# Performance work log

Hardware: AMD Instinct MI355X
Metric: run time of the kernel (lower is better)

The kernel has to match this reference:

```python
import jax, jax.numpy as jnp
import numpy as np

B, S, D, H = 2, 2048, 1024, 16
DK = D // H  # 64


def _quantum(x, W1, b1, W2, b2):
    # Stand-in for QuantumNeuralLayer: classical->quantum->classical, d_k -> d_k.
    return jnp.tanh(x @ W1 + b1) @ W2 + b2


def setup_inputs() -> dict:
    key = jax.random.key(0)
    ks = jax.random.split(key, 16)
    s = 1.0 / np.sqrt(DK)
    inp = {
        "q": jax.random.normal(ks[0], (B, S, D), dtype=jnp.float32),
        "k": jax.random.normal(ks[1], (B, S, D), dtype=jnp.float32),
        "v": jax.random.normal(ks[2], (B, S, D), dtype=jnp.float32),
    }
    names = ["q", "k", "v"]
    for i, n in enumerate(names):
        inp[f"W{n}1"] = jax.random.normal(ks[3 + 4 * i], (DK, DK), dtype=jnp.float32) * s
        inp[f"b{n}1"] = jnp.zeros((DK,), dtype=jnp.float32)
        inp[f"W{n}2"] = jax.random.normal(ks[4 + 4 * i], (DK, DK), dtype=jnp.float32) * s
        inp[f"b{n}2"] = jnp.zeros((DK,), dtype=jnp.float32)
    inp["Wo"] = jax.random.normal(ks[15], (D, D), dtype=jnp.float32) * (1.0 / np.sqrt(D))
    inp["bo"] = jnp.zeros((D,), dtype=jnp.float32)
    return inp


def reference(q, k, v, Wq1, bq1, Wq2, bq2, Wk1, bk1, Wk2, bk2,
              Wv1, bv1, Wv2, bv2, Wo, bo):
    b, s, _ = q.shape
    # split heads: [B, S, H, DK]
    qh = q.reshape(b, s, H, DK)
    kh = k.reshape(b, s, H, DK)
    vh = v.reshape(b, s, H, DK)
    # quantum per-feature transform on last dim
    qh = _quantum(qh, Wq1, bq1, Wq2, bq2)
    kh = _quantum(kh, Wk1, bk1, Wk2, bk2)
    vh = _quantum(vh, Wv1, bv1, Wv2, bv2)
    scale = 1.0 / jnp.sqrt(jnp.asarray(DK, dtype=qh.dtype))
    # scores: [B, H, S, S]
    scores = jnp.einsum("bqhd,bkhd->bhqk", qh, kh) * scale
    attn = jax.nn.softmax(scores, axis=-1)
    # context: [B, H, S, DK] -> [B, S, D]
    ctx = jnp.einsum("bhqk,bkhd->bqhd", attn, vh).reshape(b, s, D)
    return ctx @ Wo + bo
```

## Files before the change

### kernel.cpp

```cpp
#include <hip/hip_runtime.h>

#define B_ 2
#define S_ 2048
#define D_ 1024
#define H_ 16
#define DK_ 64

typedef float f32x4 __attribute__((ext_vector_type(4)));
typedef float f32x16 __attribute__((ext_vector_type(16)));
typedef short bf16x8 __attribute__((ext_vector_type(8)));

static __device__ __forceinline__ unsigned short f2bf(float f) {
  unsigned u = __float_as_uint(f);
  unsigned r = (u + 0x7FFFu + ((u >> 16) & 1u)) >> 16;
  return (unsigned short)r;
}

static __device__ __forceinline__ unsigned cvtpk_bf16(float lo, float hi) {
  unsigned r;
  asm("v_cvt_pk_bf16_f32 %0, %1, %2" : "=v"(r) : "v"(lo), "v"(hi));
  return r;
}

static __device__ __forceinline__ void load16_lds(const void* g, void* lds) {
  __builtin_amdgcn_global_load_lds(
      (const __attribute__((address_space(1))) unsigned int*)g,
      (__attribute__((address_space(3))) unsigned int*)lds, 16, 0, 0);
}

static __device__ __forceinline__ bf16x8 make_pa8(const float* p, int hi) {
  unsigned x1 = cvtpk_bf16(p[0], p[1]);
  unsigned x2 = cvtpk_bf16(p[2], p[3]);
  unsigned y1 = cvtpk_bf16(p[4], p[5]);
  unsigned y2 = cvtpk_bf16(p[6], p[7]);
  unsigned sx1 = (unsigned)__shfl_xor((int)x1, 32);
  unsigned sx2 = (unsigned)__shfl_xor((int)x2, 32);
  unsigned sy1 = (unsigned)__shfl_xor((int)y1, 32);
  unsigned sy2 = (unsigned)__shfl_xor((int)y2, 32);
  union {
    unsigned u[4];
    bf16x8 v;
  } pa;
  pa.u[0] = hi ? sy1 : x1;
  pa.u[1] = hi ? sy2 : x2;
  pa.u[2] = hi ? y1 : sx1;
  pa.u[3] = hi ? y2 : sx2;
  return pa.v;
}

static __device__ __forceinline__ float tanh_fast(float x) {
  float xc = fminf(fmaxf(x, -9.0f), 9.0f);
  float e = exp2f(xc * 2.88539008177792681472f);
  return (e - 1.0f) / (e + 1.0f);
}

__global__ __launch_bounds__(256) void quantum_fused(
    const float* __restrict__ xq, const float* __restrict__ xk,
    const float* __restrict__ xv,
    const float* __restrict__ Wq1, const float* __restrict__ bq1,
    const float* __restrict__ Wq2, const float* __restrict__ bq2,
    const float* __restrict__ Wk1, const float* __restrict__ bk1,
    const float* __restrict__ Wk2, const float* __restrict__ bk2,
    const float* __restrict__ Wv1, const float* __restrict__ bv1,
    const float* __restrict__ Wv2, const float* __restrict__ bv2,
    unsigned short* __restrict__ qhb, unsigned short* __restrict__ khb,
    unsigned short* __restrict__ vtb, float qscale) {
  const int tid = threadIdx.x;
  const int w = tid >> 6;
  const int l = tid & 63;
  const int lq = l & 31;
  const int hi = l >> 5;
  const int bh = blockIdx.y;
  const int b = bh >> 4, h = bh & 15;
  const int s0w = blockIdx.x * 128 + w * 32;

  const float* x;
  const float* W1;
  const float* b1;
  const float* W2;
  const float* b2;
  unsigned short* outp;
  float scale = 1.0f;
  int vmode = 0;
  if (blockIdx.z == 0) {
    x = xq; W1 = Wq1; b1 = bq1; W2 = Wq2; b2 = bq2; outp = qhb;
    scale = qscale;
  } else if (blockIdx.z == 1) {
    x = xk; W1 = Wk1; b1 = bk1; W2 = Wk2; b2 = bk2; outp = khb;
  } else {
    x = xv; W1 = Wv1; b1 = bv1; W2 = Wv2; b2 = bv2; outp = vtb;
    vmode = 1;
  }

  bf16x8 w1f[2][4];
#pragma unroll
  for (int ca = 0; ca < 2; ++ca)
#pragma unroll
    for (int kc = 0; kc < 4; ++kc) {
      const float* wp = W1 + (size_t)(kc * 16 + hi * 8) * 64 + ca * 32 + lq;
      union {
        unsigned u[4];
        bf16x8 v;
      } ww;
#pragma unroll
      for (int jj = 0; jj < 4; ++jj)
        ww.u[jj] = cvtpk_bf16(wp[(2 * jj) * 64], wp[(2 * jj + 1) * 64]);
      w1f[ca][kc] = ww.v;
    }

  const float* xrow = x + (((size_t)b * S_ + s0w + lq) * H_ + h) * DK_;
  bf16x8 xf[4];
#pragma unroll
  for (int kc = 0; kc < 4; ++kc) {
    float4 f0 = *(const float4*)(xrow + kc * 16 + hi * 8);
    float4 f1 = *(const float4*)(xrow + kc * 16 + hi * 8 + 4);
    union {
      unsigned u[4];
      bf16x8 v;
    } xx;
    xx.u[0] = cvtpk_bf16(f0.x, f0.y);
    xx.u[1] = cvtpk_bf16(f0.z, f0.w);
    xx.u[2] = cvtpk_bf16(f1.x, f1.y);
    xx.u[3] = cvtpk_bf16(f1.z, f1.w);
    xf[kc] = xx.v;
  }

  f32x16 acc1[2];
#pragma unroll
  for (int ca = 0; ca < 2; ++ca)
#pragma unroll
    for (int r = 0; r < 16; ++r)
      acc1[ca][r] = b1[ca * 32 + (r & 3) + 8 * (r >> 2) + 4 * hi];
#pragma unroll
  for (int kc = 0; kc < 4; ++kc) {
    acc1[0] = __builtin_amdgcn_mfma_f32_32x32x16_bf16(w1f[0][kc], xf[kc], acc1[0], 0, 0, 0);
    acc1[1] = __builtin_amdgcn_mfma_f32_32x32x16_bf16(w1f[1][kc], xf[kc], acc1[1], 0, 0, 0);
  }

  float t0[16], t1[16];
#pragma unroll
  for (int r = 0; r < 16; ++r) {
    t0[r] = tanh_fast(acc1[0][r]);
    t1[r] = tanh_fast(acc1[1][r]);
  }

  bf16x8 af[4];
  af[0] = make_pa8(&t0[0], hi);
  af[1] = make_pa8(&t0[8], hi);
  af[2] = make_pa8(&t1[0], hi);
  af[3] = make_pa8(&t1[8], hi);

  bf16x8 w2f[2][4];
#pragma unroll
  for (int nb = 0; nb < 2; ++nb)
#pragma unroll
    for (int kc = 0; kc < 4; ++kc) {
      const float* wp = W2 + (size_t)(kc * 16 + hi * 8) * 64 + nb * 32 + lq;
      union {
        unsigned u[4];
        bf16x8 v;
      } ww;
#pragma unroll
      for (int jj = 0; jj < 4; ++jj)
        ww.u[jj] = cvtpk_bf16(wp[(2 * jj) * 64], wp[(2 * jj + 1) * 64]);
      w2f[nb][kc] = ww.v;
    }

  f32x16 acc2[2];
#pragma unroll
  for (int nb = 0; nb < 2; ++nb)
#pragma unroll
    for (int r = 0; r < 16; ++r)
      acc2[nb][r] = b2[nb * 32 + (r & 3) + 8 * (r >> 2) + 4 * hi];
#pragma unroll
  for (int kc = 0; kc < 4; ++kc) {
    acc2[0] = __builtin_amdgcn_mfma_f32_32x32x16_bf16(af[kc], w2f[0][kc], acc2[0], 0, 0, 0);
    acc2[1] = __builtin_amdgcn_mfma_f32_32x32x16_bf16(af[kc], w2f[1][kc], acc2[1], 0, 0, 0);
  }

  if (!vmode) {
#pragma unroll
    for (int nb = 0; nb < 2; ++nb)
#pragma unroll
      for (int r = 0; r < 16; ++r) {
        const int s = s0w + (r & 3) + 8 * (r >> 2) + 4 * hi;
        outp[((size_t)bh * S_ + s) * DK_ + nb * 32 + lq] =
            f2bf(acc2[nb][r] * scale);
      }
  } else {
#pragma unroll
    for (int nb = 0; nb < 2; ++nb) {
      float yv[16];
#pragma unroll
      for (int r = 0; r < 16; ++r) yv[r] = acc2[nb][r];
      const size_t rowb = ((size_t)bh * DK_ + nb * 32 + lq) * S_;
      *(bf16x8*)(outp + rowb + s0w + hi * 8) = make_pa8(&yv[0], hi);
      *(bf16x8*)(outp + rowb + s0w + 16 + hi * 8) = make_pa8(&yv[8], hi);
    }
  }
}

__global__ __launch_bounds__(256, 2) void attn_kernel(
    const unsigned short* __restrict__ qhb,
    const unsigned short* __restrict__ khb,
    const unsigned short* __restrict__ vtb,
    unsigned short* __restrict__ ctxb) {
  __shared__ __align__(16) unsigned short ks_u[64 * 64];
  __shared__ __align__(16) unsigned short vs_u[64 * 64];

  const int tid = threadIdx.x;
  const int w = tid >> 6;
  const int l = tid & 63;
  const int lq = l & 31;
  const int hi = l >> 5;
  const int bh = blockIdx.x;
  const int b = bh >> 4, h = bh & 15;
  const int q0 = blockIdx.y * 128 + w * 32;

  const unsigned short* qp = qhb + ((size_t)bh * S_ + q0 + lq) * DK_ + hi * 8;
  bf16x8 qf[4];
#pragma unroll
  for (int kc = 0; kc < 4; ++kc) qf[kc] = *(const bf16x8*)(qp + kc * 16);

  f32x16 o0 = {}, o1 = {};
  float m_ = -1e30f, l_ = 0.f;

  const int kk = tid >> 2, ch = tid & 3;
  const unsigned short* kgbase = khb + (size_t)bh * S_ * DK_;
  const unsigned short* vgbase = vtb + (size_t)bh * DK_ * S_;

  for (int t0 = 0; t0 < S_; t0 += 64) {
    __syncthreads();
    {
      const uint4* gk = (const uint4*)(kgbase + ((size_t)(t0 + kk)) * DK_ + ch * 16);
      uint4 a0 = gk[0];
      uint4 a1 = gk[1];
      char* kd = (char*)ks_u + kk * 128;
      *(uint4*)(kd + (((ch * 2 + 0) ^ (kk & 7)) << 4)) = a0;
      *(uint4*)(kd + (((ch * 2 + 1) ^ (kk & 7)) << 4)) = a1;

      const uint4* gv = (const uint4*)(vgbase + ((size_t)kk) * S_ + t0 + ch * 16);
      uint4 b0 = gv[0];
      uint4 b1 = gv[1];
      char* vd = (char*)vs_u + kk * 128;
      *(uint4*)(vd + (((ch * 2 + 0) ^ (kk & 7)) << 4)) = b0;
      *(uint4*)(vd + (((ch * 2 + 1) ^ (kk & 7)) << 4)) = b1;
    }
    __syncthreads();

    f32x16 s0 = {}, s1 = {};
#pragma unroll
    for (int kc = 0; kc < 4; ++kc) {
      const int slot = kc * 2 + hi;
      bf16x8 k0 = *(const bf16x8*)((const char*)ks_u + lq * 128 +
                                   ((slot ^ (lq & 7)) << 4));
      bf16x8 k1 = *(const bf16x8*)((const char*)ks_u + (32 + lq) * 128 +
                                   ((slot ^ (lq & 7)) << 4));
      s0 = __builtin_amdgcn_mfma_f32_32x32x16_bf16(k0, qf[kc], s0, 0, 0, 0);
      s1 = __builtin_amdgcn_mfma_f32_32x32x16_bf16(k1, qf[kc], s1, 0, 0, 0);
    }

    float pmax = s0[0];
#pragma unroll
    for (int i = 1; i < 16; ++i) pmax = fmaxf(pmax, s0[i]);
#pragma unroll
    for (int i = 0; i < 16; ++i) pmax = fmaxf(pmax, s1[i]);
    pmax = fmaxf(pmax, __shfl_xor(pmax, 32));

    if (!__all(pmax <= m_ + 8.0f)) {
      const float mnew = fmaxf(m_, pmax);
      const float scl = exp2f(m_ - mnew);
      m_ = mnew;
      l_ *= scl;
#pragma unroll
      for (int r = 0; r < 16; ++r) {
        const float sr = __shfl(scl, ((r & 3) + 8 * (r >> 2)) + 4 * hi);
        o0[r] *= sr;
        o1[r] *= sr;
      }
    }

    float p0[16], p1[16];
#pragma unroll
    for (int i = 0; i < 16; ++i) p0[i] = exp2f(s0[i] - m_);
#pragma unroll
    for (int i = 0; i < 16; ++i) p1[i] = exp2f(s1[i] - m_);
    float ps = 0.f;
    {
      float t0a = 0.f, t1a = 0.f, t2a = 0.f, t3a = 0.f;
#pragma unroll
      for (int i = 0; i < 16; i += 4) {
        t0a += p0[i] + p1[i];
        t1a += p0[i + 1] + p1[i + 1];
        t2a += p0[i + 2] + p1[i + 2];
        t3a += p0[i + 3] + p1[i + 3];
      }
      ps = (t0a + t1a) + (t2a + t3a);
    }
    ps += __shfl_xor(ps, 32);
    l_ += ps;

    union {
      unsigned u[4];
      bf16x8 v;
    } pa;

#define MAKE_PA(PARR, CC)                                            \
  {                                                                  \
    unsigned x1 = cvtpk_bf16(PARR[(CC)*8 + 0], PARR[(CC)*8 + 1]);    \
    unsigned x2 = cvtpk_bf16(PARR[(CC)*8 + 2], PARR[(CC)*8 + 3]);    \
    unsigned y1 = cvtpk_bf16(PARR[(CC)*8 + 4], PARR[(CC)*8 + 5]);    \
    unsigned y2 = cvtpk_bf16(PARR[(CC)*8 + 6], PARR[(CC)*8 + 7]);    \
    unsigned sx1 = (unsigned)__shfl_xor((int)x1, 32);                \
    unsigned sx2 = (unsigned)__shfl_xor((int)x2, 32);                \
    unsigned sy1 = (unsigned)__shfl_xor((int)y1, 32);                \
    unsigned sy2 = (unsigned)__shfl_xor((int)y2, 32);                \
    pa.u[0] = hi ? sy1 : x1;                                         \
    pa.u[1] = hi ? sy2 : x2;                                         \
    pa.u[2] = hi ? y1 : sx1;                                         \
    pa.u[3] = hi ? y2 : sx2;                                         \
  }

#define PV_STEP(CIDX)                                                         \
  {                                                                           \
    const int slot = (CIDX)*2 + hi;                                           \
    bf16x8 v0 = *(const bf16x8*)((const char*)vs_u + lq * 128 +               \
                                 ((slot ^ (lq & 7)) << 4));                   \
    bf16x8 v1 = *(const bf16x8*)((const char*)vs_u + (32 + lq) * 128 +        \
                                 ((slot ^ (lq & 7)) << 4));                   \
    o0 = __builtin_amdgcn_mfma_f32_32x32x16_bf16(pa.v, v0, o0, 0, 0, 0);      \
    o1 = __builtin_amdgcn_mfma_f32_32x32x16_bf16(pa.v, v1, o1, 0, 0, 0);      \
  }

    MAKE_PA(p0, 0) PV_STEP(0)
    MAKE_PA(p0, 1) PV_STEP(1)
    MAKE_PA(p1, 0) PV_STEP(2)
    MAKE_PA(p1, 1) PV_STEP(3)
#undef MAKE_PA
#undef PV_STEP
  }

  const float linv = 1.0f / l_;
#pragma unroll
  for (int r = 0; r < 16; ++r) {
    const int crow = ((r & 3) + 8 * (r >> 2)) + 4 * hi;
    const float lr = __shfl(linv, crow);
    const int qg = q0 + crow;
    const size_t base = ((size_t)b * S_ + qg) * D_ + h * DK_;
    ctxb[base + lq] = f2bf(o0[r] * lr);
    ctxb[base + 32 + lq] = f2bf(o1[r] * lr);
  }
}

__global__ __launch_bounds__(256) void wo_transpose(
    const float* __restrict__ Wo, unsigned short* __restrict__ WoT) {
  __shared__ float t[64][65];
  const int k0 = blockIdx.x * 64, n0 = blockIdx.y * 64;
  const int r = threadIdx.x >> 4, c4 = threadIdx.x & 15;
#pragma unroll
  for (int i = 0; i < 4; ++i) {
    float4 v = *(const float4*)&Wo[(size_t)(k0 + r + 16 * i) * D_ + n0 + c4 * 4];
    t[r + 16 * i][c4 * 4 + 0] = v.x;
    t[r + 16 * i][c4 * 4 + 1] = v.y;
    t[r + 16 * i][c4 * 4 + 2] = v.z;
    t[r + 16 * i][c4 * 4 + 3] = v.w;
  }
  __syncthreads();
  const int n = threadIdx.x >> 2, kc = threadIdx.x & 3;
  union {
    unsigned short u[16];
    uint4 v[2];
  } pk;
#pragma unroll
  for (int j = 0; j < 16; ++j) pk.u[j] = f2bf(t[kc * 16 + j][n]);
  unsigned short* op = WoT + (size_t)(n0 + n) * D_ + k0 + kc * 16;
  *(uint4*)op = pk.v[0];
  *(uint4*)(op + 8) = pk.v[1];
}

__global__ __launch_bounds__(256) void out_gemm_mfma(
    const unsigned short* __restrict__ A,
    const unsigned short* __restrict__ BT,
    const float* __restrict__ bo, float* __restrict__ C) {
  __shared__ __align__(16) unsigned short As[128 * 64];
  __shared__ __align__(16) unsigned short Bs[128 * 64];

  const int tid = threadIdx.x;
  const int w = tid >> 6, l = tid & 63;
  const int ll = l & 15, lg = l >> 4;
  const int wr = w >> 1, wc = w & 1;
  const int m0 = blockIdx.y * 128, n0 = blockIdx.x * 128;

  const int srow = l >> 3;
  const int sslot = (l & 7) ^ srow;
  const int g_off = sslot * 8;

  f32x4 acc[4][4];
#pragma unroll
  for (int mt = 0; mt < 4; ++mt)
#pragma unroll
    for (int nt = 0; nt < 4; ++nt) acc[mt][nt] = (f32x4){0.f, 0.f, 0.f, 0.f};

  for (int k0 = 0; k0 < D_; k0 += 64) {
    __syncthreads();
#pragma unroll
    for (int c = 0; c < 4; ++c) {
      const int row = c * 32 + w * 8 + srow;
      load16_lds(A + (size_t)(m0 + row) * D_ + k0 + g_off,
                 (char*)As + c * 4096 + w * 1024);
      load16_lds(BT + (size_t)(n0 + row) * D_ + k0 + g_off,
                 (char*)Bs + c * 4096 + w * 1024);
    }
    __syncthreads();

#pragma unroll
    for (int half = 0; half < 2; ++half) {
      bf16x8 af[4], bfr[4];
#pragma unroll
      for (int mt = 0; mt < 4; ++mt) {
        const int row = wr * 64 + mt * 16 + ll;
        af[mt] = *(const bf16x8*)((const char*)As + row * 128 +
                                  (((half * 4 + lg) ^ (row & 7)) << 4));
      }
#pragma unroll
      for (int nt = 0; nt < 4; ++nt) {
        const int rowb = wc * 64 + nt * 16 + ll;
        bfr[nt] = *(const bf16x8*)((const char*)Bs + rowb * 128 +
                                   (((half * 4 + lg) ^ (rowb & 7)) << 4));
      }
#pragma unroll
      for (int mt = 0; mt < 4; ++mt)
#pragma unroll
        for (int nt = 0; nt < 4; ++nt)
          acc[mt][nt] = __builtin_amdgcn_mfma_f32_16x16x32_bf16(
              af[mt], bfr[nt], acc[mt][nt], 0, 0, 0);
    }
  }

#pragma unroll
  for (int nt = 0; nt < 4; ++nt) {
    const int col = n0 + wc * 64 + nt * 16 + ll;
    const float bv = bo[col];
#pragma unroll
    for (int mt = 0; mt < 4; ++mt) {
      const int row0 = m0 + wr * 64 + mt * 16 + lg * 4;
#pragma unroll
      for (int r = 0; r < 4; ++r)
        C[(size_t)(row0 + r) * D_ + col] = acc[mt][nt][r] + bv;
    }
  }
}

extern "C" void kernel_launch(void* const* d_in, const int* in_sizes, int n_in,
                              void* d_out, int out_size, void* d_ws,
                              size_t ws_size, hipStream_t stream) {
  const float* q = (const float*)d_in[0];
  const float* k = (const float*)d_in[1];
  const float* v = (const float*)d_in[2];
  const float* Wq1 = (const float*)d_in[3];
  const float* bq1 = (const float*)d_in[4];
  const float* Wq2 = (const float*)d_in[5];
  const float* bq2 = (const float*)d_in[6];
  const float* Wk1 = (const float*)d_in[7];
  const float* bk1 = (const float*)d_in[8];
  const float* Wk2 = (const float*)d_in[9];
  const float* bk2 = (const float*)d_in[10];
  const float* Wv1 = (const float*)d_in[11];
  const float* bv1 = (const float*)d_in[12];
  const float* Wv2 = (const float*)d_in[13];
  const float* bv2 = (const float*)d_in[14];
  const float* Wo = (const float*)d_in[15];
  const float* bo = (const float*)d_in[16];
  float* out = (float*)d_out;

  const size_t TEN = (size_t)B_ * H_ * S_ * DK_;
  char* ws = (char*)d_ws;
  unsigned short* qhb = (unsigned short*)ws;
  unsigned short* khb = (unsigned short*)(ws + TEN * 2);
  unsigned short* vtb = (unsigned short*)(ws + TEN * 4);
  unsigned short* ctxb = (unsigned short*)(ws + TEN * 6);
  unsigned short* wot = (unsigned short*)(ws + TEN * 8);

  const float cs = 0.125f * 1.44269504088896340736f;
  quantum_fused<<<dim3(16, 32, 3), 256, 0, stream>>>(
      q, k, v, Wq1, bq1, Wq2, bq2, Wk1, bk1, Wk2, bk2, Wv1, bv1, Wv2, bv2,
      qhb, khb, vtb, cs);
  wo_transpose<<<dim3(16, 16), 256, 0, stream>>>(Wo, wot);

  attn_kernel<<<dim3(32, 16), 256, 0, stream>>>(qhb, khb, vtb, ctxb);

  out_gemm_mfma<<<dim3(8, 32), 256, 0, stream>>>(ctxb, wot, bo, out);
}
```

Baseline: 116.6 us.

## Split KV sequence across wave pairs in attention and merge partial softmax

The attention kernel now gives each block 64 queries, twice as many blocks, and splits the key/value sequence into two halves, each handled by one pair of waves with its own LDS tiles. Partial outputs and (max, sum) statistics are merged through LDS at the end. K/V loads for the next tile are issued into registers before the current tile's compute to overlap global latency, and occupancy is raised to 4 blocks per CU. In exchange there are extra barriers per tile, an LDS-based final merge, and higher register pressure under the tighter launch bound.

```diff
diff --git a/kernel.cpp b/kernel.cpp
--- a/kernel.cpp
+++ b/kernel.cpp
@@ -200,22 +200,23 @@
   }
 }
 
-__global__ __launch_bounds__(256, 2) void attn_kernel(
+__global__ __launch_bounds__(256, 4) void attn_kernel(
     const unsigned short* __restrict__ qhb,
     const unsigned short* __restrict__ khb,
     const unsigned short* __restrict__ vtb,
     unsigned short* __restrict__ ctxb) {
-  __shared__ __align__(16) unsigned short ks_u[64 * 64];
-  __shared__ __align__(16) unsigned short vs_u[64 * 64];
+  __shared__ __align__(16) unsigned short ks_u[2][64 * 64];
+  __shared__ __align__(16) unsigned short vs_u[2][64 * 64];
 
   const int tid = threadIdx.x;
   const int w = tid >> 6;
+  const int p = w >> 1;
   const int l = tid & 63;
   const int lq = l & 31;
   const int hi = l >> 5;
   const int bh = blockIdx.x;
   const int b = bh >> 4, h = bh & 15;
-  const int q0 = blockIdx.y * 128 + w * 32;
+  const int q0 = blockIdx.y * 64 + (w & 1) * 32;
 
   const unsigned short* qp = qhb + ((size_t)bh * S_ + q0 + lq) * DK_ + hi * 8;
   bf16x8 qf[4];
@@ -225,37 +226,48 @@
   f32x16 o0 = {}, o1 = {};
   float m_ = -1e30f, l_ = 0.f;
 
-  const int kk = tid >> 2, ch = tid & 3;
+  const int kk = (tid & 127) >> 1;
+  const int ch2 = tid & 1;
   const unsigned short* kgbase = khb + (size_t)bh * S_ * DK_;
   const unsigned short* vgbase = vtb + (size_t)bh * DK_ * S_;
-
-  for (int t0 = 0; t0 < S_; t0 += 64) {
-    __syncthreads();
-    {
-      const uint4* gk = (const uint4*)(kgbase + ((size_t)(t0 + kk)) * DK_ + ch * 16);
-      uint4 a0 = gk[0];
-      uint4 a1 = gk[1];
-      char* kd = (char*)ks_u + kk * 128;
-      *(uint4*)(kd + (((ch * 2 + 0) ^ (kk & 7)) << 4)) = a0;
-      *(uint4*)(kd + (((ch * 2 + 1) ^ (kk & 7)) << 4)) = a1;
-
-      const uint4* gv = (const uint4*)(vgbase + ((size_t)kk) * S_ + t0 + ch * 16);
-      uint4 b0 = gv[0];
-      uint4 b1 = gv[1];
-      char* vd = (char*)vs_u + kk * 128;
-      *(uint4*)(vd + (((ch * 2 + 0) ^ (kk & 7)) << 4)) = b0;
-      *(uint4*)(vd + (((ch * 2 + 1) ^ (kk & 7)) << 4)) = b1;
-    }
-    __syncthreads();
+  char* ksP = (char*)&ks_u[p][0];
+  char* vsP = (char*)&vs_u[p][0];
+
+  uint4 ra[4], rb[4];
+
+#define LOADKV(TT)                                                            \
+  {                                                                           \
+    const int tb = p * 1024 + (TT)*64;                                        \
+    const uint4* gk =                                                         \
+        (const uint4*)(kgbase + (size_t)(tb + kk) * DK_ + ch2 * 32);          \
+    ra[0] = gk[0]; ra[1] = gk[1]; ra[2] = gk[2]; ra[3] = gk[3];               \
+    const uint4* gv = (const uint4*)(vgbase + (size_t)kk * S_ + tb + ch2 * 32);\
+    rb[0] = gv[0]; rb[1] = gv[1]; rb[2] = gv[2]; rb[3] = gv[3];               \
+  }
+
+#define WRITEKV()                                                             \
+  {                                                                           \
+    char* kd = ksP + kk * 128;                                                \
+    char* vd = vsP + kk * 128;                                                \
+    _Pragma("unroll") for (int j = 0; j < 4; ++j) {                           \
+      *(uint4*)(kd + (((ch2 * 4 + j) ^ (kk & 7)) << 4)) = ra[j];              \
+      *(uint4*)(vd + (((ch2 * 4 + j) ^ (kk & 7)) << 4)) = rb[j];              \
+    }                                                                         \
+  }
+
+  LOADKV(0)
+  WRITEKV()
+  __syncthreads();
+
+  for (int t = 0; t < 16; ++t) {
+    if (t < 15) LOADKV(t + 1)
 
     f32x16 s0 = {}, s1 = {};
 #pragma unroll
     for (int kc = 0; kc < 4; ++kc) {
       const int slot = kc * 2 + hi;
-      bf16x8 k0 = *(const bf16x8*)((const char*)ks_u + lq * 128 +
-                                   ((slot ^ (lq & 7)) << 4));
-      bf16x8 k1 = *(const bf16x8*)((const char*)ks_u + (32 + lq) * 128 +
-                                   ((slot ^ (lq & 7)) << 4));
+      bf16x8 k0 = *(const bf16x8*)(ksP + lq * 128 + ((slot ^ (lq & 7)) << 4));
+      bf16x8 k1 = *(const bf16x8*)(ksP + (32 + lq) * 128 + ((slot ^ (lq & 7)) << 4));
       s0 = __builtin_amdgcn_mfma_f32_32x32x16_bf16(k0, qf[kc], s0, 0, 0, 0);
       s1 = __builtin_amdgcn_mfma_f32_32x32x16_bf16(k1, qf[kc], s1, 0, 0, 0);
     }
@@ -280,75 +292,92 @@
       }
     }
 
-    float p0[16], p1[16];
-#pragma unroll
-    for (int i = 0; i < 16; ++i) p0[i] = exp2f(s0[i] - m_);
-#pragma unroll
-    for (int i = 0; i < 16; ++i) p1[i] = exp2f(s1[i] - m_);
-    float ps = 0.f;
+#pragma unroll
+    for (int i = 0; i < 16; ++i) s0[i] = exp2f(s0[i] - m_);
+#pragma unroll
+    for (int i = 0; i < 16; ++i) s1[i] = exp2f(s1[i] - m_);
     {
       float t0a = 0.f, t1a = 0.f, t2a = 0.f, t3a = 0.f;
 #pragma unroll
       for (int i = 0; i < 16; i += 4) {
-        t0a += p0[i] + p1[i];
-        t1a += p0[i + 1] + p1[i + 1];
-        t2a += p0[i + 2] + p1[i + 2];
-        t3a += p0[i + 3] + p1[i + 3];
+        t0a += s0[i] + s1[i];
+        t1a += s0[i + 1] + s1[i + 1];
+        t2a += s0[i + 2] + s1[i + 2];
+        t3a += s0[i + 3] + s1[i + 3];
       }
-      ps = (t0a + t1a) + (t2a + t3a);
-    }
-    ps += __shfl_xor(ps, 32);
-    l_ += ps;
-
+      float ps = (t0a + t1a) + (t2a + t3a);
+      ps += __shfl_xor(ps, 32);
+      l_ += ps;
+    }
+
+    float pv[8];
     union {
       unsigned u[4];
       bf16x8 v;
     } pa;
 
-#define MAKE_PA(PARR, CC)                                            \
-  {                                                                  \
-    unsigned x1 = cvtpk_bf16(PARR[(CC)*8 + 0], PARR[(CC)*8 + 1]);    \
-    unsigned x2 = cvtpk_bf16(PARR[(CC)*8 + 2], PARR[(CC)*8 + 3]);    \
-    unsigned y1 = cvtpk_bf16(PARR[(CC)*8 + 4], PARR[(CC)*8 + 5]);    \
-    unsigned y2 = cvtpk_bf16(PARR[(CC)*8 + 6], PARR[(CC)*8 + 7]);    \
-    unsigned sx1 = (unsigned)__shfl_xor((int)x1, 32);                \
-    unsigned sx2 = (unsigned)__shfl_xor((int)x2, 32);                \
-    unsigned sy1 = (unsigned)__shfl_xor((int)y1, 32);                \
-    unsigned sy2 = (unsigned)__shfl_xor((int)y2, 32);                \
-    pa.u[0] = hi ? sy1 : x1;                                         \
-    pa.u[1] = hi ? sy2 : x2;                                         \
-    pa.u[2] = hi ? y1 : sx1;                                         \
-    pa.u[3] = hi ? y2 : sx2;                                         \
-  }
-
-#define PV_STEP(CIDX)                                                         \
+#define PV_STEP(SARR, CC, CIDX)                                               \
   {                                                                           \
+    _Pragma("unroll") for (int j = 0; j < 8; ++j) pv[j] = SARR[(CC)*8 + j];   \
+    pa.v = make_pa8(pv, hi);                                                  \
     const int slot = (CIDX)*2 + hi;                                           \
-    bf16x8 v0 = *(const bf16x8*)((const char*)vs_u + lq * 128 +               \
-                                 ((slot ^ (lq & 7)) << 4));                   \
-    bf16x8 v1 = *(const bf16x8*)((const char*)vs_u + (32 + lq) * 128 +        \
-                                 ((slot ^ (lq & 7)) << 4));                   \
+    bf16x8 v0 = *(const bf16x8*)(vsP + lq * 128 + ((slot ^ (lq & 7)) << 4));  \
+    bf16x8 v1 = *(const bf16x8*)(vsP + (32 + lq) * 128 + ((slot ^ (lq & 7)) << 4)); \
     o0 = __builtin_amdgcn_mfma_f32_32x32x16_bf16(pa.v, v0, o0, 0, 0, 0);      \
     o1 = __builtin_amdgcn_mfma_f32_32x32x16_bf16(pa.v, v1, o1, 0, 0, 0);      \
   }
 
-    MAKE_PA(p0, 0) PV_STEP(0)
-    MAKE_PA(p0, 1) PV_STEP(1)
-    MAKE_PA(p1, 0) PV_STEP(2)
-    MAKE_PA(p1, 1) PV_STEP(3)
-#undef MAKE_PA
+    PV_STEP(s0, 0, 0)
+    PV_STEP(s0, 1, 1)
+    PV_STEP(s1, 0, 2)
+    PV_STEP(s1, 1, 3)
 #undef PV_STEP
-  }
-
-  const float linv = 1.0f / l_;
-#pragma unroll
-  for (int r = 0; r < 16; ++r) {
-    const int crow = ((r & 3) + 8 * (r >> 2)) + 4 * hi;
-    const float lr = __shfl(linv, crow);
-    const int qg = q0 + crow;
-    const size_t base = ((size_t)b * S_ + qg) * D_ + h * DK_;
-    ctxb[base + lq] = f2bf(o0[r] * lr);
-    ctxb[base + 32 + lq] = f2bf(o1[r] * lr);
+
+    __syncthreads();
+    if (t < 15) WRITEKV()
+    __syncthreads();
+  }
+#undef LOADKV
+#undef WRITEKV
+
+  float* ksf = (float*)&ks_u[0][0];
+  float* mlf = (float*)&vs_u[0][0];
+  const int qlb = (w & 1) * 32;
+
+  if (p == 1) {
+#pragma unroll
+    for (int r = 0; r < 16; ++r) {
+      const int ql = qlb + (r & 3) + 8 * (r >> 2) + 4 * hi;
+      ksf[ql * 64 + lq] = o0[r];
+      ksf[ql * 64 + 32 + lq] = o1[r];
+    }
+    if (l < 32) {
+      mlf[(qlb + lq) * 2] = m_;
+      mlf[(qlb + lq) * 2 + 1] = l_;
+    }
+  } else {
+    if (l < 32) {
+      mlf[128 + (qlb + lq) * 2] = m_;
+      mlf[128 + (qlb + lq) * 2 + 1] = l_;
+    }
+  }
+  __syncthreads();
+
+  if (p == 0) {
+#pragma unroll
+    for (int r = 0; r < 16; ++r) {
+      const int ql = qlb + (r & 3) + 8 * (r >> 2) + 4 * hi;
+      const float mB = mlf[ql * 2], lB = mlf[ql * 2 + 1];
+      const float mA = mlf[128 + ql * 2], lA = mlf[128 + ql * 2 + 1];
+      const float mm = fmaxf(mA, mB);
+      const float al = exp2f(mA - mm), be = exp2f(mB - mm);
+      const float li = 1.0f / (lA * al + lB * be);
+      const float fa = al * li, fb = be * li;
+      const int qg = blockIdx.y * 64 + ql;
+      const size_t base = ((size_t)b * S_ + qg) * D_ + h * DK_;
+      ctxb[base + lq] = f2bf(o0[r] * fa + ksf[ql * 64 + lq] * fb);
+      ctxb[base + 32 + lq] = f2bf(o1[r] * fa + ksf[ql * 64 + 32 + lq] * fb);
+    }
   }
 }
 
@@ -487,7 +516,7 @@
       qhb, khb, vtb, cs);
   wo_transpose<<<dim3(16, 16), 256, 0, stream>>>(Wo, wot);
 
-  attn_kernel<<<dim3(32, 16), 256, 0, stream>>>(qhb, khb, vtb, ctxb);
+  attn_kernel<<<dim3(32, 32), 256, 0, stream>>>(qhb, khb, vtb, ctxb);
 
   out_gemm_mfma<<<dim3(8, 32), 256, 0, stream>>>(ctxb, wot, bo, out);
 }
```

After: 221.9 us. 90.3% more time.
